# Optimization experiments

Measured on AMD Instinct MI355X. Metric: run time of the kernel, lower is better.

## Reference

```python
import jax, jax.numpy as jnp
import numpy as np

N, INSIZE, K, D = 512, 512, 64, 16


def setup_inputs() -> dict:
    key = jax.random.key(0)
    k1, k2, k3 = jax.random.split(key, 3)
    x = jax.random.normal(k1, (N, INSIZE), dtype=jnp.float32)
    W = jax.random.normal(k2, (K * D, INSIZE), dtype=jnp.float32) * (1.0 / np.sqrt(INSIZE))
    b = jax.random.normal(k3, (K * D,), dtype=jnp.float32) * 0.01
    return {"x": x, "W": W, "b": b}


def reference(x, W, b):
    # Linear: [N, insize] -> [N, K*D] -> [N, K, D]
    feat = (x @ W.T + b).reshape(-1, K, D)
    n = feat.shape[0]
    # Pairwise L1 distance over D: norm[i, k, j] = sum_d |feat[i,k,d] - feat[j,k,d]|
    # feature [N,K,D,1] vs feature_ [1,K,D,N] in the original broadcast
    diff = jnp.abs(feat[:, :, :, None] - jnp.transpose(feat, (1, 2, 0))[None])  # [N,K,D,N]
    norm = jnp.sum(diff, axis=2)  # [N,K,N]
    # Eraser: suppress self-similarity on the diagonal with a large penalty
    eraser = jnp.eye(n, dtype=feat.dtype)[:, None, :]  # [N,1,N]
    c_b = jnp.exp(-(norm + eraser * 1e6))
    o_b = jnp.sum(c_b, axis=2)  # [N,K]
    return jnp.concatenate((x, o_b), axis=1)  # [N, insize+K]
```

## Files before the change

kernel.cpp:

```cpp
#include <hip/hip_runtime.h>

#define NPTS 512
#define INS  512
#define KDIM 64
#define DDIM 16
#define CDIM (KDIM*DDIM)
#define OUTC (INS + KDIM)
#define KSPLIT 4
#define FEAT_ELEMS ((size_t)NPTS * CDIM)

__device__ __forceinline__ float exp2_fast(float x) {
    return __builtin_amdgcn_exp2f(x);
}

__global__ __launch_bounds__(256) void gemm_kernel(
    const float* __restrict__ x,
    const float* __restrict__ W,
    const float* __restrict__ bias,
    float* __restrict__ featT)
{
    const int tid = threadIdx.x;
    const int cbase = blockIdx.x * 64;
    const int ibase = blockIdx.y * 32;
    const int kbase = blockIdx.z * (INS / KSPLIT);

    __shared__ float xs[16][32 + 2];
    __shared__ float wss[16][64 + 4];

    const int tx = tid & 15;
    const int ty = tid >> 4;

    float acc[2][4] = {};

    const int kkL = tid & 15;
    const int rL  = tid >> 4;

    for (int k0 = kbase; k0 < kbase + INS / KSPLIT; k0 += 16) {
        xs[kkL][rL]      = x[(ibase + rL) * INS + k0 + kkL];
        xs[kkL][rL + 16] = x[(ibase + rL + 16) * INS + k0 + kkL];
        wss[kkL][rL]      = W[(cbase + rL) * INS + k0 + kkL];
        wss[kkL][rL + 16] = W[(cbase + rL + 16) * INS + k0 + kkL];
        wss[kkL][rL + 32] = W[(cbase + rL + 32) * INS + k0 + kkL];
        wss[kkL][rL + 48] = W[(cbase + rL + 48) * INS + k0 + kkL];
        __syncthreads();

        #pragma unroll
        for (int kk = 0; kk < 16; ++kk) {
            float2 a = *(const float2*)&xs[kk][ty * 2];
            float4 w = *(const float4*)&wss[kk][tx * 4];
            acc[0][0] += a.x * w.x;  acc[0][1] += a.x * w.y;
            acc[0][2] += a.x * w.z;  acc[0][3] += a.x * w.w;
            acc[1][0] += a.y * w.x;  acc[1][1] += a.y * w.y;
            acc[1][2] += a.y * w.z;  acc[1][3] += a.y * w.w;
        }
        __syncthreads();
    }

    const float LOG2E = 1.4426950408889634f;
    const float bsel = (blockIdx.z == 0) ? 1.0f : 0.0f;
    const int c = cbase + tx * 4;
    float4 bq = *(const float4*)&bias[c];
    const int k = c >> 4;
    const int d = c & 15;
    float* dst = featT + (size_t)blockIdx.z * FEAT_ELEMS;
    #pragma unroll
    for (int ii = 0; ii < 2; ++ii) {
        const int i = ibase + ty * 2 + ii;
        float4 v;
        v.x = (acc[ii][0] + bq.x * bsel) * LOG2E;
        v.y = (acc[ii][1] + bq.y * bsel) * LOG2E;
        v.z = (acc[ii][2] + bq.z * bsel) * LOG2E;
        v.w = (acc[ii][3] + bq.w * bsel) * LOG2E;
        *(float4*)&dst[((size_t)k * NPTS + i) * DDIM + d] = v;
    }
}

__global__ __launch_bounds__(256) void init_out_kernel(
    const float* __restrict__ x, float* __restrict__ out)
{
    const int idx = blockIdx.x * 256 + threadIdx.x;
    const int i  = idx / (OUTC / 4);
    const int j4 = idx - i * (OUTC / 4);
    float4 v;
    if (j4 < INS / 4) {
        v = ((const float4*)x)[i * (INS / 4) + j4];
    } else {
        v = make_float4(-1.0f, -1.0f, -1.0f, -1.0f);
    }
    ((float4*)out)[idx] = v;
}

__device__ __forceinline__ void load_feat16(
    const float* f0, const float* f1, const float* f2, const float* f3,
    size_t off, float* fi)
{
    #pragma unroll
    for (int q = 0; q < 4; ++q) {
        float4 a = *(const float4*)(f0 + off + q * 4);
        float4 b = *(const float4*)(f1 + off + q * 4);
        float4 c = *(const float4*)(f2 + off + q * 4);
        float4 d = *(const float4*)(f3 + off + q * 4);
        fi[q * 4 + 0] = (a.x + b.x) + (c.x + d.x);
        fi[q * 4 + 1] = (a.y + b.y) + (c.y + d.y);
        fi[q * 4 + 2] = (a.z + b.z) + (c.z + d.z);
        fi[q * 4 + 3] = (a.w + b.w) + (c.w + d.w);
    }
}

__global__ __launch_bounds__(256, 4) void pairwise_kernel(
    const float* __restrict__ f0, const float* __restrict__ f1,
    const float* __restrict__ f2, const float* __restrict__ f3,
    float* __restrict__ out)
{
    const int k     = blockIdx.x;
    const int itile = blockIdx.y;
    const int jq    = blockIdx.z;

    __shared__ float fj[128 * DDIM];
    __shared__ float part[4][128];

    {
        const size_t base = ((size_t)k * NPTS + jq * 128) * DDIM;
        const float4* s0 = (const float4*)(f0 + base);
        const float4* s1 = (const float4*)(f1 + base);
        const float4* s2 = (const float4*)(f2 + base);
        const float4* s3 = (const float4*)(f3 + base);
        float4* dst = (float4*)fj;
        #pragma unroll
        for (int u = 0; u < 2; ++u) {
            int idx = threadIdx.x + u * 256;
            float4 a = s0[idx], b = s1[idx], c = s2[idx], d = s3[idx];
            float4 r;
            r.x = (a.x + b.x) + (c.x + d.x);
            r.y = (a.y + b.y) + (c.y + d.y);
            r.z = (a.z + b.z) + (c.z + d.z);
            r.w = (a.w + b.w) + (c.w + d.w);
            dst[idx] = r;
        }
    }

    const int lane = threadIdx.x & 63;
    const int wv   = threadIdx.x >> 6;
    const int i0   = itile * 128 + lane;
    const int i1   = i0 + 64;

    float fi0[16], fi1[16];
    load_feat16(f0, f1, f2, f3, ((size_t)k * NPTS + i0) * DDIM, fi0);
    load_feat16(f0, f1, f2, f3, ((size_t)k * NPTS + i1) * DDIM, fi1);
    __syncthreads();

    float acc0 = 0.f, acc1 = 0.f;
    const float* fp = fj + wv * 32 * DDIM;
    #pragma unroll 2
    for (int jj = 0; jj < 32; ++jj) {
        const float* p = fp + jj * DDIM;
        float4 q0 = *(const float4*)(p);
        float4 q1 = *(const float4*)(p + 4);
        float4 q2 = *(const float4*)(p + 8);
        float4 q3 = *(const float4*)(p + 12);
        {
            float a0 = fabsf(fi0[0]  - q0.x) + fabsf(fi0[1]  - q0.y)
                     + fabsf(fi0[2]  - q0.z) + fabsf(fi0[3]  - q0.w);
            float a1 = fabsf(fi0[4]  - q1.x) + fabsf(fi0[5]  - q1.y)
                     + fabsf(fi0[6]  - q1.z) + fabsf(fi0[7]  - q1.w);
            float a2 = fabsf(fi0[8]  - q2.x) + fabsf(fi0[9]  - q2.y)
                     + fabsf(fi0[10] - q2.z) + fabsf(fi0[11] - q2.w);
            float a3 = fabsf(fi0[12] - q3.x) + fabsf(fi0[13] - q3.y)
                     + fabsf(fi0[14] - q3.z) + fabsf(fi0[15] - q3.w);
            acc0 += exp2_fast(-((a0 + a1) + (a2 + a3)));
        }
        {
            float b0 = fabsf(fi1[0]  - q0.x) + fabsf(fi1[1]  - q0.y)
                     + fabsf(fi1[2]  - q0.z) + fabsf(fi1[3]  - q0.w);
            float b1 = fabsf(fi1[4]  - q1.x) + fabsf(fi1[5]  - q1.y)
                     + fabsf(fi1[6]  - q1.z) + fabsf(fi1[7]  - q1.w);
            float b2 = fabsf(fi1[8]  - q2.x) + fabsf(fi1[9]  - q2.y)
                     + fabsf(fi1[10] - q2.z) + fabsf(fi1[11] - q2.w);
            float b3 = fabsf(fi1[12] - q3.x) + fabsf(fi1[13] - q3.y)
                     + fabsf(fi1[14] - q3.z) + fabsf(fi1[15] - q3.w);
            acc1 += exp2_fast(-((b0 + b1) + (b2 + b3)));
        }
    }

    part[wv][lane]      = acc0;
    part[wv][lane + 64] = acc1;
    __syncthreads();

    if (threadIdx.x < 128) {
        float s = (part[0][threadIdx.x] + part[1][threadIdx.x])
                + (part[2][threadIdx.x] + part[3][threadIdx.x]);
        const int i = itile * 128 + threadIdx.x;
        atomicAdd(&out[(size_t)i * OUTC + INS + k], s);
    }
}

extern "C" void kernel_launch(void* const* d_in, const int* in_sizes, int n_in,
                              void* d_out, int out_size, void* d_ws, size_t ws_size,
                              hipStream_t stream) {
    const float* x    = (const float*)d_in[0];
    const float* W    = (const float*)d_in[1];
    const float* bias = (const float*)d_in[2];
    float* out = (float*)d_out;
    float* featT = (float*)d_ws;

    gemm_kernel<<<dim3(CDIM / 64, NPTS / 32, KSPLIT), 256, 0, stream>>>(x, W, bias, featT);
    init_out_kernel<<<dim3(NPTS * (OUTC / 4) / 256), 256, 0, stream>>>(x, out);
    pairwise_kernel<<<dim3(KDIM, 4, 4), 256, 0, stream>>>(
        featT, featT + FEAT_ELEMS, featT + 2 * FEAT_ELEMS, featT + 3 * FEAT_ELEMS, out);
}
```

Measured before the change: 97.70 us.

## Replace FP32 split-K GEMM with split-bf16 MFMA GEMM and single feature buffer

Adds a conversion kernel that splits x and W into high and low bf16 parts, and replaces the scalar FP32 split-K GEMM with an MFMA bf16 GEMM that uses three products (hh, hl, lh) to approximate FP32 accuracy. Because split-K is gone, the pairwise kernel reads one feature buffer instead of summing four partials. This removes the slow FP32 FMA GEMM and the extra partial-sum traffic. The cost is an extra conversion launch, more workspace, and a small precision loss that the exp of large L1 distances may amplify.

```diff
diff --git a/kernel.cpp b/kernel.cpp
--- a/kernel.cpp
+++ b/kernel.cpp
@@ -6,72 +6,141 @@
 #define DDIM 16
 #define CDIM (KDIM*DDIM)
 #define OUTC (INS + KDIM)
-#define KSPLIT 4
-#define FEAT_ELEMS ((size_t)NPTS * CDIM)
+
+typedef __attribute__((ext_vector_type(4))) float f32x4;
+typedef __attribute__((ext_vector_type(8))) short short8v;
+typedef __attribute__((ext_vector_type(4))) unsigned short u16x4;
+typedef __attribute__((ext_vector_type(8))) unsigned short u16x8;
 
 __device__ __forceinline__ float exp2_fast(float x) {
     return __builtin_amdgcn_exp2f(x);
 }
 
-__global__ __launch_bounds__(256) void gemm_kernel(
-    const float* __restrict__ x,
-    const float* __restrict__ W,
+__device__ __forceinline__ unsigned short f2bf_rne(float f) {
+    unsigned u = __float_as_uint(f);
+    u += 0x7FFF + ((u >> 16) & 1);
+    return (unsigned short)(u >> 16);
+}
+__device__ __forceinline__ float bf2f(unsigned short h) {
+    return __uint_as_float(((unsigned)h) << 16);
+}
+
+__global__ __launch_bounds__(256) void convert_kernel(
+    const float* __restrict__ x, const float* __restrict__ W,
+    unsigned short* __restrict__ xh, unsigned short* __restrict__ xl,
+    unsigned short* __restrict__ wh, unsigned short* __restrict__ wl)
+{
+    const int gid = blockIdx.x * 256 + threadIdx.x;
+    const float4* src;
+    unsigned short *dh, *dl;
+    int idx;
+    if (gid < NPTS * INS / 4) {
+        src = (const float4*)x; idx = gid; dh = xh; dl = xl;
+    } else {
+        src = (const float4*)W; idx = gid - NPTS * INS / 4; dh = wh; dl = wl;
+    }
+    float4 v = src[idx];
+    u16x4 hv, lv;
+    hv[0] = f2bf_rne(v.x); lv[0] = f2bf_rne(v.x - bf2f(hv[0]));
+    hv[1] = f2bf_rne(v.y); lv[1] = f2bf_rne(v.y - bf2f(hv[1]));
+    hv[2] = f2bf_rne(v.z); lv[2] = f2bf_rne(v.z - bf2f(hv[2]));
+    hv[3] = f2bf_rne(v.w); lv[3] = f2bf_rne(v.w - bf2f(hv[3]));
+    *(u16x4*)&dh[idx * 4] = hv;
+    *(u16x4*)&dl[idx * 4] = lv;
+}
+
+#define BM 64
+#define BN 64
+#define BK 32
+#define LDK 40
+
+__global__ __launch_bounds__(256) void gemm_mfma_kernel(
+    const unsigned short* __restrict__ xh, const unsigned short* __restrict__ xl,
+    const unsigned short* __restrict__ wh, const unsigned short* __restrict__ wl,
     const float* __restrict__ bias,
     float* __restrict__ featT)
 {
-    const int tid = threadIdx.x;
-    const int cbase = blockIdx.x * 64;
-    const int ibase = blockIdx.y * 32;
-    const int kbase = blockIdx.z * (INS / KSPLIT);
-
-    __shared__ float xs[16][32 + 2];
-    __shared__ float wss[16][64 + 4];
-
-    const int tx = tid & 15;
-    const int ty = tid >> 4;
-
-    float acc[2][4] = {};
-
-    const int kkL = tid & 15;
-    const int rL  = tid >> 4;
-
-    for (int k0 = kbase; k0 < kbase + INS / KSPLIT; k0 += 16) {
-        xs[kkL][rL]      = x[(ibase + rL) * INS + k0 + kkL];
-        xs[kkL][rL + 16] = x[(ibase + rL + 16) * INS + k0 + kkL];
-        wss[kkL][rL]      = W[(cbase + rL) * INS + k0 + kkL];
-        wss[kkL][rL + 16] = W[(cbase + rL + 16) * INS + k0 + kkL];
-        wss[kkL][rL + 32] = W[(cbase + rL + 32) * INS + k0 + kkL];
-        wss[kkL][rL + 48] = W[(cbase + rL + 48) * INS + k0 + kkL];
+    __shared__ unsigned short Ah[BM * LDK], Al[BM * LDK];
+    __shared__ unsigned short Bh[BN * LDK], Bl[BN * LDK];
+
+    const int tid   = threadIdx.x;
+    const int cbase = blockIdx.x * BN;
+    const int ibase = blockIdx.y * BM;
+
+    const int lane = tid & 63;
+    const int wv   = tid >> 6;
+    const int wm   = wv >> 1;
+    const int wn   = wv & 1;
+
+    const int srow = tid >> 2;
+    const int skg  = tid & 3;
+    const size_t gA0 = (size_t)(ibase + srow) * INS + skg * 8;
+    const size_t gB0 = (size_t)(cbase + srow) * INS + skg * 8;
+    const int    loff = srow * LDK + skg * 8;
+
+    const int frow  = lane & 15;
+    const int fg    = lane >> 4;
+    const int aoff  = (wm * 32 + frow) * LDK + fg * 8;
+    const int boff  = (wn * 32 + frow) * LDK + fg * 8;
+
+    f32x4 acc[2][2] = {};
+
+    u16x8 ra = *(const u16x8*)&xh[gA0];
+    u16x8 rl = *(const u16x8*)&xl[gA0];
+    u16x8 rb = *(const u16x8*)&wh[gB0];
+    u16x8 rc = *(const u16x8*)&wl[gB0];
+
+    for (int kt = 0; kt < INS / BK; ++kt) {
         __syncthreads();
-
-        #pragma unroll
-        for (int kk = 0; kk < 16; ++kk) {
-            float2 a = *(const float2*)&xs[kk][ty * 2];
-            float4 w = *(const float4*)&wss[kk][tx * 4];
-            acc[0][0] += a.x * w.x;  acc[0][1] += a.x * w.y;
-            acc[0][2] += a.x * w.z;  acc[0][3] += a.x * w.w;
-            acc[1][0] += a.y * w.x;  acc[1][1] += a.y * w.y;
-            acc[1][2] += a.y * w.z;  acc[1][3] += a.y * w.w;
-        }
+        *(u16x8*)&Ah[loff] = ra;
+        *(u16x8*)&Al[loff] = rl;
+        *(u16x8*)&Bh[loff] = rb;
+        *(u16x8*)&Bl[loff] = rc;
         __syncthreads();
+        if (kt + 1 < INS / BK) {
+            const size_t o = (size_t)(kt + 1) * BK;
+            ra = *(const u16x8*)&xh[gA0 + o];
+            rl = *(const u16x8*)&xl[gA0 + o];
+            rb = *(const u16x8*)&wh[gB0 + o];
+            rc = *(const u16x8*)&wl[gB0 + o];
+        }
+
+        short8v ah[2], al[2], bh[2], bl[2];
+        #pragma unroll
+        for (int f = 0; f < 2; ++f) {
+            ah[f] = *(const short8v*)&Ah[aoff + f * 16 * LDK];
+            al[f] = *(const short8v*)&Al[aoff + f * 16 * LDK];
+            bh[f] = *(const short8v*)&Bh[boff + f * 16 * LDK];
+            bl[f] = *(const short8v*)&Bl[boff + f * 16 * LDK];
+        }
+        #pragma unroll
+        for (int m = 0; m < 2; ++m) {
+            #pragma unroll
+            for (int n = 0; n < 2; ++n) {
+                acc[m][n] = __builtin_amdgcn_mfma_f32_16x16x32_bf16(ah[m], bh[n], acc[m][n], 0, 0, 0);
+                acc[m][n] = __builtin_amdgcn_mfma_f32_16x16x32_bf16(ah[m], bl[n], acc[m][n], 0, 0, 0);
+                acc[m][n] = __builtin_amdgcn_mfma_f32_16x16x32_bf16(al[m], bh[n], acc[m][n], 0, 0, 0);
+            }
+        }
     }
 
     const float LOG2E = 1.4426950408889634f;
-    const float bsel = (blockIdx.z == 0) ? 1.0f : 0.0f;
-    const int c = cbase + tx * 4;
-    float4 bq = *(const float4*)&bias[c];
-    const int k = c >> 4;
-    const int d = c & 15;
-    float* dst = featT + (size_t)blockIdx.z * FEAT_ELEMS;
+    const int r0 = (lane >> 4) * 4;
     #pragma unroll
-    for (int ii = 0; ii < 2; ++ii) {
-        const int i = ibase + ty * 2 + ii;
-        float4 v;
-        v.x = (acc[ii][0] + bq.x * bsel) * LOG2E;
-        v.y = (acc[ii][1] + bq.y * bsel) * LOG2E;
-        v.z = (acc[ii][2] + bq.z * bsel) * LOG2E;
-        v.w = (acc[ii][3] + bq.w * bsel) * LOG2E;
-        *(float4*)&dst[((size_t)k * NPTS + i) * DDIM + d] = v;
+    for (int m = 0; m < 2; ++m) {
+        const int i0 = ibase + wm * 32 + m * 16 + r0;
+        #pragma unroll
+        for (int n = 0; n < 2; ++n) {
+            const int c  = cbase + wn * 32 + n * 16 + (lane & 15);
+            const float bv = bias[c];
+            const int kk = c >> 4;
+            const int d  = c & 15;
+            float* dst = featT + (size_t)kk * NPTS * DDIM + d;
+            #pragma unroll
+            for (int r = 0; r < 4; ++r) {
+                dst[(size_t)(i0 + r) * DDIM] = (acc[m][n][r] + bv) * LOG2E;
+            }
+        }
     }
 }
 
@@ -90,27 +159,8 @@
     ((float4*)out)[idx] = v;
 }
 
-__device__ __forceinline__ void load_feat16(
-    const float* f0, const float* f1, const float* f2, const float* f3,
-    size_t off, float* fi)
-{
-    #pragma unroll
-    for (int q = 0; q < 4; ++q) {
-        float4 a = *(const float4*)(f0 + off + q * 4);
-        float4 b = *(const float4*)(f1 + off + q * 4);
-        float4 c = *(const float4*)(f2 + off + q * 4);
-        float4 d = *(const float4*)(f3 + off + q * 4);
-        fi[q * 4 + 0] = (a.x + b.x) + (c.x + d.x);
-        fi[q * 4 + 1] = (a.y + b.y) + (c.y + d.y);
-        fi[q * 4 + 2] = (a.z + b.z) + (c.z + d.z);
-        fi[q * 4 + 3] = (a.w + b.w) + (c.w + d.w);
-    }
-}
-
 __global__ __launch_bounds__(256, 4) void pairwise_kernel(
-    const float* __restrict__ f0, const float* __restrict__ f1,
-    const float* __restrict__ f2, const float* __restrict__ f3,
-    float* __restrict__ out)
+    const float* __restrict__ f0, float* __restrict__ out)
 {
     const int k     = blockIdx.x;
     const int itile = blockIdx.y;
@@ -122,21 +172,9 @@
     {
         const size_t base = ((size_t)k * NPTS + jq * 128) * DDIM;
         const float4* s0 = (const float4*)(f0 + base);
-        const float4* s1 = (const float4*)(f1 + base);
-        const float4* s2 = (const float4*)(f2 + base);
-        const float4* s3 = (const float4*)(f3 + base);
         float4* dst = (float4*)fj;
-        #pragma unroll
-        for (int u = 0; u < 2; ++u) {
-            int idx = threadIdx.x + u * 256;
-            float4 a = s0[idx], b = s1[idx], c = s2[idx], d = s3[idx];
-            float4 r;
-            r.x = (a.x + b.x) + (c.x + d.x);
-            r.y = (a.y + b.y) + (c.y + d.y);
-            r.z = (a.z + b.z) + (c.z + d.z);
-            r.w = (a.w + b.w) + (c.w + d.w);
-            dst[idx] = r;
-        }
+        dst[threadIdx.x]       = s0[threadIdx.x];
+        dst[threadIdx.x + 256] = s0[threadIdx.x + 256];
     }
 
     const int lane = threadIdx.x & 63;
@@ -145,8 +183,19 @@
     const int i1   = i0 + 64;
 
     float fi0[16], fi1[16];
-    load_feat16(f0, f1, f2, f3, ((size_t)k * NPTS + i0) * DDIM, fi0);
-    load_feat16(f0, f1, f2, f3, ((size_t)k * NPTS + i1) * DDIM, fi1);
+    {
+        const float4* p0 = (const float4*)(f0 + ((size_t)k * NPTS + i0) * DDIM);
+        const float4* p1 = (const float4*)(f0 + ((size_t)k * NPTS + i1) * DDIM);
+        #pragma unroll
+        for (int q = 0; q < 4; ++q) {
+            float4 a = p0[q];
+            fi0[q * 4 + 0] = a.x; fi0[q * 4 + 1] = a.y;
+            fi0[q * 4 + 2] = a.z; fi0[q * 4 + 3] = a.w;
+            float4 b = p1[q];
+            fi1[q * 4 + 0] = b.x; fi1[q * 4 + 1] = b.y;
+            fi1[q * 4 + 2] = b.z; fi1[q * 4 + 3] = b.w;
+        }
+    }
     __syncthreads();
 
     float acc0 = 0.f, acc1 = 0.f;
@@ -201,10 +250,17 @@
     const float* W    = (const float*)d_in[1];
     const float* bias = (const float*)d_in[2];
     float* out = (float*)d_out;
+
     float* featT = (float*)d_ws;
-
-    gemm_kernel<<<dim3(CDIM / 64, NPTS / 32, KSPLIT), 256, 0, stream>>>(x, W, bias, featT);
+    unsigned short* xh = (unsigned short*)((char*)d_ws + (size_t)(2 << 20));
+    unsigned short* xl = xh + (size_t)NPTS * INS;
+    unsigned short* wh = xl + (size_t)NPTS * INS;
+    unsigned short* wl = wh + (size_t)CDIM * INS;
+
+    convert_kernel<<<dim3((NPTS * INS / 4 + CDIM * INS / 4) / 256), 256, 0, stream>>>(
+        x, W, xh, xl, wh, wl);
+    gemm_mfma_kernel<<<dim3(CDIM / BN, NPTS / BM), 256, 0, stream>>>(
+        xh, xl, wh, wl, bias, featT);
     init_out_kernel<<<dim3(NPTS * (OUTC / 4) / 256), 256, 0, stream>>>(x, out);
-    pairwise_kernel<<<dim3(KDIM, 4, 4), 256, 0, stream>>>(
-        featT, featT + FEAT_ELEMS, featT + 2 * FEAT_ELEMS, featT + 3 * FEAT_ELEMS, out);
-}
+    pairwise_kernel<<<dim3(KDIM, 4, 4), 256, 0, stream>>>(featT, out);
+}
```

Measured after the change: 94.77 us. 3.0% less time.
